# Kernel tuning notes

Hardware: AMD Instinct MI355X
Metric: run time of the kernel (lower is better)

Reference implementation:

```python
import jax, jax.numpy as jnp
import numpy as np

NCE_T = 0.07


def setup_inputs() -> dict:
    key = jax.random.key(0)
    k1, k2, k3 = jax.random.split(key, 3)
    features_1 = jax.random.normal(k1, (1, 20000, 256), dtype=jnp.float32)
    features_2 = jax.random.normal(k2, (1, 8192, 256), dtype=jnp.float32)
    map21 = jax.random.randint(k3, (8192,), 0, 20000, dtype=jnp.int64)
    return {"features_1": features_1, "features_2": features_2, "map21": map21}


def reference(features_1, features_2, map21):
    # squeeze leading batch dim (module assumes batch size 1)
    f1 = features_1[0]  # [N1, D]
    f2 = features_2[0]  # [P, D]  (P == nce_num_pairs == len(map21) -> arange branch)
    query = f1[map21]   # [P, D] gather
    keys = f2           # [P, D]
    # pairwise Euclidean distance via matmul trick (matches torch.cdist p=2)
    q_sq = jnp.sum(query * query, axis=-1)  # [P]
    k_sq = jnp.sum(keys * keys, axis=-1)    # [P]
    sq_dist = q_sq[:, None] + k_sq[None, :] - 2.0 * (query @ keys.T)  # [P, P]
    dist = jnp.sqrt(jnp.maximum(sq_dist, 0.0))
    logits = -dist / NCE_T
    # cross entropy with labels = arange(P): mean of -log_softmax diagonal
    logp = jax.nn.log_softmax(logits, axis=-1)
    loss = -jnp.mean(jnp.diagonal(logp))
    return loss
```

## Files before the change

kernel.cpp:

```cpp
#include <hip/hip_runtime.h>
#include <hip/hip_bf16.h>

#define PP      8192
#define DIM     256
#define DIMP    272
#define NKF     17
#define GS      (32 * DIMP)
#define NCHUNK  16
#define TCOLS   16
#define ROWBLK  256
#define NROWBLK (PP / ROWBLK)
#define TILEB   (32 * DIMP * 2)
#define NBUF    2

typedef __bf16 bf16_t;
using bf16x8 = __attribute__((ext_vector_type(8))) __bf16;
using bf16x4 = __attribute__((ext_vector_type(4))) __bf16;
using f32x4  = __attribute__((ext_vector_type(4))) float;
using f32x16 = __attribute__((ext_vector_type(16))) float;

typedef __attribute__((address_space(1))) void as1_void;
typedef __attribute__((address_space(3))) void as3_void;

#define C2    20.609929155556618
#define MEXP  (-340.0f)
#define COEF  ((float)(-(C2 * 1.4142135623730951) * 8388608.0))
#define KBIAS ((float)((127.0 + 340.0) * 8388608.0))
#define LN2   0.6931471805599453f

__global__ __launch_bounds__(256) void nce_prep(
    const float* __restrict__ f1, const float* __restrict__ f2,
    const int* __restrict__ map,
    bf16_t* __restrict__ qb2, bf16_t* __restrict__ kb2,
    float* __restrict__ diag2, float* __restrict__ part_l,
    unsigned* __restrict__ cnt, float* __restrict__ out)
{
    const int tid  = threadIdx.x;
    const int wave = tid >> 6, lane = tid & 63;
    const int p    = blockIdx.x * 4 + wave;
    const int gtid = blockIdx.x * 256 + tid;

    if (gtid < PP) part_l[gtid] = 0.0f;
    if (gtid < NROWBLK) cnt[gtid] = 0u;
    if (gtid == 0) out[0] = 0.0f;

    const int idx = map[p];
    const f32x4 qv = *(const f32x4*)(f1 + (size_t)idx * DIM + lane * 4);
    const f32x4 kv = *(const f32x4*)(f2 + (size_t)p * DIM + lane * 4);

    float qs = qv[0]*qv[0] + qv[1]*qv[1] + qv[2]*qv[2] + qv[3]*qv[3];
    float ks = kv[0]*kv[0] + kv[1]*kv[1] + kv[2]*kv[2] + kv[3]*kv[3];
    const f32x4 dv = qv - kv;
    float ds = dv[0]*dv[0] + dv[1]*dv[1] + dv[2]*dv[2] + dv[3]*dv[3];

    bf16x4 qo, ko;
    #pragma unroll
    for (int i = 0; i < 4; ++i) { qo[i] = (bf16_t)qv[i]; ko[i] = (bf16_t)kv[i]; }

    const int G = p >> 5, l31 = p & 31;
    const int kk = lane >> 2, h = (lane >> 1) & 1, j0 = (lane & 1) * 4;
    const size_t base = (size_t)G * GS;
    const size_t off  = base + (size_t)(kk * 64 + h * 32 + l31) * 8 + j0;
    *(bf16x4*)(qb2 + off) = qo;
    *(bf16x4*)(kb2 + off) = ko;

    #pragma unroll
    for (int s = 32; s > 0; s >>= 1) {
        qs += __shfl_xor(qs, s);
        ks += __shfl_xor(ks, s);
        ds += __shfl_xor(ds, s);
    }

    if (lane < 4) {
        const int hh = lane & 1;
        bf16x8 v;
        #pragma unroll
        for (int i = 0; i < 8; ++i) v[i] = (bf16_t)0.0f;
        if (lane == 0) {
            const float qh = -0.5f * qs;
            const bf16_t q1 = (bf16_t)qh;
            v[0] = q1; v[1] = (bf16_t)(qh - (float)q1);
            v[2] = (bf16_t)1.0f; v[3] = (bf16_t)1.0f;
        } else if (lane == 2) {
            const float kh = -0.5f * ks;
            const bf16_t k1 = (bf16_t)kh;
            v[0] = (bf16_t)1.0f; v[1] = (bf16_t)1.0f;
            v[2] = k1; v[3] = (bf16_t)(kh - (float)k1);
        }
        bf16_t* dstp = (lane < 2) ? qb2 : kb2;
        *(bf16x8*)(dstp + base + (size_t)(1024 + hh * 32 + l31) * 8) = v;
    }
    if (lane == 0)
        diag2[p] = (float)(-C2) * __builtin_amdgcn_sqrtf(ds);
}

__device__ __forceinline__ void stage(const bf16_t* __restrict__ kb2,
                                      int Gc, int wave, int lane, char* dst)
{
    __builtin_assume(wave >= 0 && wave < 4);
    __builtin_assume(lane >= 0 && lane < 64);
    const bf16_t* src = kb2 + (size_t)Gc * GS + wave * 512 + lane * 8;
    char* d = dst + wave * 1024;
    #pragma unroll
    for (int j = 0; j < 4; ++j)
        __builtin_amdgcn_global_load_lds((const as1_void*)(src + j * 2048),
                                         (as3_void*)(d + j * 4096), 16, 0, 0);
    if (wave == 0)
        __builtin_amdgcn_global_load_lds((const as1_void*)(src + 4 * 2048),
                                         (as3_void*)(d + 4 * 4096), 16, 0, 0);
}

#define PHASE(NW, DOPRE, T)                                                    \
  do {                                                                         \
    asm volatile("s_waitcnt lgkmcnt(0)\n\ts_barrier" ::: "memory");            \
    if (DOPRE) stage(kb2, c0g + (T) + 1, wave, lane, smem[((T) + 1) & 1]);     \
    asm volatile("s_waitcnt vmcnt(%c0)" :: "i"(NW) : "memory");                \
    const bf16_t* bp = (const bf16_t*)smem[(T) & 1] + lane * 8;                \
    f32x16 acc0 = {0,0,0,0,0,0,0,0,0,0,0,0,0,0,0,0};                          \
    f32x16 acc1 = {0,0,0,0,0,0,0,0,0,0,0,0,0,0,0,0};                          \
    __builtin_amdgcn_s_setprio(1);                                             \
    _Pragma("unroll")                                                          \
    for (int kk = 0; kk < NKF; ++kk) {                                         \
        const bf16x8 b = *(const bf16x8*)(bp + kk * 512);                      \
        acc0 = __builtin_amdgcn_mfma_f32_32x32x16_bf16(a0[kk], b, acc0,0,0,0); \
        acc1 = __builtin_amdgcn_mfma_f32_32x32x16_bf16(a1[kk], b, acc1,0,0,0); \
    }                                                                          \
    __builtin_amdgcn_s_setprio(0);                                             \
         \
    _Pragma("unroll")                                                          \
    for (int i = 0; i < 16; ++i) {                                             \
        const float t0 = __builtin_amdgcn_sqrtf(-acc0[i]);                     \
        const float u0 = fmaxf(fmaf(t0, COEF, KBIAS), 0.0f);                   \
        l0[i] += __uint_as_float((unsigned)u0);                                \
        const float t1 = __builtin_amdgcn_sqrtf(-acc1[i]);                     \
        const float u1 = fmaxf(fmaf(t1, COEF, KBIAS), 0.0f);                   \
        l1[i] += __uint_as_float((unsigned)u1);                                \
    }                                                                          \
  } while (0)

__global__ __launch_bounds__(256, 2) void nce_main(
    const bf16_t* __restrict__ qb2, const bf16_t* __restrict__ kb2,
    const float* __restrict__ diag2, float* __restrict__ part_l,
    unsigned* __restrict__ cnt, float* __restrict__ out)
{
    const int tid  = threadIdx.x, wave = tid >> 6, lane = tid & 63;
    const int l31  = lane & 31, h = lane >> 5;

    const int lin = blockIdx.x + (blockIdx.y << 5);
    const int xcd = lin & 7, idx = lin >> 3;
    const int rb  = (xcd & 3) * 8 + (idx & 7);
    const int cy  = (xcd >> 2) * 8 + (idx >> 3);
    const int G0  = rb * 8 + wave * 2;
    const int c0g = cy * TCOLS;

    __shared__ __align__(16) char smem[NBUF][TILEB];
    __shared__ int s_last;
    __shared__ float red[4];

    stage(kb2, c0g, wave, lane, smem[0]);

    bf16x8 a0[NKF], a1[NKF];
    {
        const bf16_t* ap0 = qb2 + (size_t)G0 * GS + lane * 8;
        const bf16_t* ap1 = ap0 + GS;
        #pragma unroll
        for (int kk = 0; kk < NKF; ++kk) {
            a0[kk] = *(const bf16x8*)(ap0 + kk * 512);
            a1[kk] = *(const bf16x8*)(ap1 + kk * 512);
        }
    }

    float l0[16], l1[16];
    #pragma unroll
    for (int i = 0; i < 16; ++i) { l0[i] = 0.0f; l1[i] = 0.0f; }

    #pragma unroll 1
    for (int t = 0; t < TCOLS - 1; ++t)
        PHASE(4, true, t);
    PHASE(0, false, TCOLS - 1);

    #pragma unroll
    for (int s = 1; s < 32; s <<= 1) {
        #pragma unroll
        for (int i = 0; i < 16; ++i) {
            l0[i] += __shfl_xor(l0[i], s);
            l1[i] += __shfl_xor(l1[i], s);
        }
    }

    if (l31 == 0) {
        #pragma unroll
        for (int i = 0; i < 16; ++i) {
            const int r = (i & 3) + 8 * (i >> 2) + 4 * h;
            atomicAdd(&part_l[G0 * 32 + r], l0[i]);
            atomicAdd(&part_l[(G0 + 1) * 32 + r], l1[i]);
        }
    }

    __syncthreads();
    if (tid == 0) {
        __threadfence();
        s_last = (atomicAdd(&cnt[rb], 1u) == NCHUNK - 1) ? 1 : 0;
    }
    __syncthreads();
    if (s_last) {
        const int row = rb * ROWBLK + tid;
        const float lf = atomicAdd(&part_l[row], 0.0f);
        float v = MEXP + __builtin_amdgcn_logf(lf) - diag2[row];
        #pragma unroll
        for (int s = 1; s < 64; s <<= 1) v += __shfl_xor(v, s);
        if (lane == 0) red[wave] = v;
        __syncthreads();
        if (tid == 0)
            atomicAdd(out, (red[0] + red[1] + red[2] + red[3]) * (LN2 / (float)PP));
    }
}

extern "C" void kernel_launch(void* const* d_in, const int* in_sizes, int n_in,
                              void* d_out, int out_size, void* d_ws, size_t ws_size,
                              hipStream_t stream)
{
    const float* f1  = (const float*)d_in[0];
    const float* f2  = (const float*)d_in[1];
    const int*   map = (const int*)d_in[2];
    float* out = (float*)d_out;

    char* ws = (char*)d_ws;
    bf16_t*   qb2    = (bf16_t*)ws;
    bf16_t*   kb2    = qb2 + (size_t)256 * GS;
    float*    diag2  = (float*)(ws + 2ull * 256 * GS * sizeof(bf16_t));
    float*    part_l = diag2 + PP;
    unsigned* cnt    = (unsigned*)(part_l + PP);

    nce_prep<<<PP / 4, 256, 0, stream>>>(f1, f2, map, qb2, kb2, diag2,
                                         part_l, cnt, out);
    nce_main<<<dim3(NROWBLK, NCHUNK), 256, 0, stream>>>(qb2, kb2, diag2,
                                                        part_l, cnt, out);
}
```

Before: 120.3 us.

## Software-pipeline MFMA and epilogue across tiles with split accumulators

Restructures the column-tile loop so the MFMA chain for tile t runs in the same phase as the sqrt/softmax epilogue of tile t-1, using double-buffered accumulator sets. Each tile's K reduction is split into even and odd accumulator chains to shorten the MFMA dependency chain, and the two chains are summed in the epilogue. Launch bounds drop to one block per SIMD group to make room for the extra accumulator registers. The cost is a much higher register footprint, lower occupancy, and a full vmcnt(0) wait at each barrier instead of a partial one.

```diff
diff --git a/kernel.cpp b/kernel.cpp
--- a/kernel.cpp
+++ b/kernel.cpp
@@ -110,35 +110,49 @@
                                          (as3_void*)(d + 4 * 4096), 16, 0, 0);
 }
 
-#define PHASE(NW, DOPRE, T)                                                    \
+#define PH_MFMA(T, Pe0, Po0, Pe1, Po1)                                         \
   do {                                                                         \
-    asm volatile("s_waitcnt lgkmcnt(0)\n\ts_barrier" ::: "memory");            \
-    if (DOPRE) stage(kb2, c0g + (T) + 1, wave, lane, smem[((T) + 1) & 1]);     \
-    asm volatile("s_waitcnt vmcnt(%c0)" :: "i"(NW) : "memory");                \
     const bf16_t* bp = (const bf16_t*)smem[(T) & 1] + lane * 8;                \
-    f32x16 acc0 = {0,0,0,0,0,0,0,0,0,0,0,0,0,0,0,0};                          \
-    f32x16 acc1 = {0,0,0,0,0,0,0,0,0,0,0,0,0,0,0,0};                          \
+    bf16x8 be = *(const bf16x8*)(bp);                                          \
+    bf16x8 bo = *(const bf16x8*)(bp + 512);                                    \
     __builtin_amdgcn_s_setprio(1);                                             \
+    Pe0 = __builtin_amdgcn_mfma_f32_32x32x16_bf16(a0[0], be, ZZ, 0, 0, 0);     \
+    Pe1 = __builtin_amdgcn_mfma_f32_32x32x16_bf16(a1[0], be, ZZ, 0, 0, 0);     \
+    Po0 = __builtin_amdgcn_mfma_f32_32x32x16_bf16(a0[1], bo, ZZ, 0, 0, 0);     \
+    Po1 = __builtin_amdgcn_mfma_f32_32x32x16_bf16(a1[1], bo, ZZ, 0, 0, 0);     \
     _Pragma("unroll")                                                          \
-    for (int kk = 0; kk < NKF; ++kk) {                                         \
-        const bf16x8 b = *(const bf16x8*)(bp + kk * 512);                      \
-        acc0 = __builtin_amdgcn_mfma_f32_32x32x16_bf16(a0[kk], b, acc0,0,0,0); \
-        acc1 = __builtin_amdgcn_mfma_f32_32x32x16_bf16(a1[kk], b, acc1,0,0,0); \
+    for (int kk = 2; kk < NKF; kk += 2) {                                      \
+        be = *(const bf16x8*)(bp + kk * 512);                                  \
+        Pe0 = __builtin_amdgcn_mfma_f32_32x32x16_bf16(a0[kk], be, Pe0,0,0,0);  \
+        Pe1 = __builtin_amdgcn_mfma_f32_32x32x16_bf16(a1[kk], be, Pe1,0,0,0);  \
+        if (kk + 1 < NKF) {                                                    \
+            bo = *(const bf16x8*)(bp + (kk + 1) * 512);                        \
+            Po0 = __builtin_amdgcn_mfma_f32_32x32x16_bf16(a0[kk+1], bo, Po0,0,0,0); \
+            Po1 = __builtin_amdgcn_mfma_f32_32x32x16_bf16(a1[kk+1], bo, Po1,0,0,0); \
+        }                                                                      \
     }                                                                          \
     __builtin_amdgcn_s_setprio(0);                                             \
-         \
+  } while (0)
+
+#define EPI(Pe0, Po0, Pe1, Po1)                                                \
+  do {                                                                         \
     _Pragma("unroll")                                                          \
     for (int i = 0; i < 16; ++i) {                                             \
-        const float t0 = __builtin_amdgcn_sqrtf(-acc0[i]);                     \
+        const float s0 = Pe0[i] + Po0[i];                                      \
+        const float t0 = __builtin_amdgcn_sqrtf(-s0);                          \
         const float u0 = fmaxf(fmaf(t0, COEF, KBIAS), 0.0f);                   \
         l0[i] += __uint_as_float((unsigned)u0);                                \
-        const float t1 = __builtin_amdgcn_sqrtf(-acc1[i]);                     \
+        const float s1 = Pe1[i] + Po1[i];                                      \
+        const float t1 = __builtin_amdgcn_sqrtf(-s1);                          \
         const float u1 = fmaxf(fmaf(t1, COEF, KBIAS), 0.0f);                   \
         l1[i] += __uint_as_float((unsigned)u1);                                \
     }                                                                          \
   } while (0)
 
-__global__ __launch_bounds__(256, 2) void nce_main(
+#define PH_BOT() \
+    asm volatile("s_waitcnt vmcnt(0) lgkmcnt(0)\n\ts_barrier" ::: "memory")
+
+__global__ __launch_bounds__(256, 1) void nce_main(
     const bf16_t* __restrict__ qb2, const bf16_t* __restrict__ kb2,
     const float* __restrict__ diag2, float* __restrict__ part_l,
     unsigned* __restrict__ cnt, float* __restrict__ out)
@@ -174,10 +188,30 @@
     #pragma unroll
     for (int i = 0; i < 16; ++i) { l0[i] = 0.0f; l1[i] = 0.0f; }
 
+    const f32x16 ZZ = {0,0,0,0,0,0,0,0,0,0,0,0,0,0,0,0};
+    f32x16 pe0, po0, pe1, po1;
+    f32x16 qe0, qo0, qe1, qo1;
+
+    PH_BOT();
+
+    stage(kb2, c0g + 1, wave, lane, smem[1]);
+    PH_MFMA(0, pe0, po0, pe1, po1);
+    PH_BOT();
+
     #pragma unroll 1
-    for (int t = 0; t < TCOLS - 1; ++t)
-        PHASE(4, true, t);
-    PHASE(0, false, TCOLS - 1);
+    for (int tt = 1; tt <= 13; tt += 2) {
+        stage(kb2, c0g + tt + 1, wave, lane, smem[(tt + 1) & 1]);
+        PH_MFMA(tt, qe0, qo0, qe1, qo1);
+        EPI(pe0, po0, pe1, po1);
+        PH_BOT();
+        stage(kb2, c0g + tt + 2, wave, lane, smem[tt & 1]);
+        PH_MFMA(tt + 1, pe0, po0, pe1, po1);
+        EPI(qe0, qo0, qe1, qo1);
+        PH_BOT();
+    }
+    PH_MFMA(15, qe0, qo0, qe1, qo1);
+    EPI(pe0, po0, pe1, po1);
+    EPI(qe0, qo0, qe1, qo1);
 
     #pragma unroll
     for (int s = 1; s < 32; s <<= 1) {
```

Measured after the change: 131.0 us. +8.9%, slower.

## Software-pipeline MFMA tiles with deferred epilogue and split even/odd accumulators

Applied to the files above, without the earlier changes.

Restructures each column-tile phase so that the sqrt/clamp epilogue for the previous tile runs interleaved between MFMA groups of the current tile. It also splits each accumulator into even and odd chains to shorten MFMA dependency chains, and prefetches B fragments from LDS in batches. The waitcnt/barrier moves to the end of each phase. Launch bounds drop to one block per CU so the doubled accumulator registers fit, which trades occupancy for instruction-level parallelism.

```diff
diff --git a/kernel.cpp b/kernel.cpp
--- a/kernel.cpp
+++ b/kernel.cpp
@@ -110,35 +110,68 @@
                                          (as3_void*)(d + 4 * 4096), 16, 0, 0);
 }
 
-#define PHASE(NW, DOPRE, T)                                                    \
-  do {                                                                         \
-    asm volatile("s_waitcnt lgkmcnt(0)\n\ts_barrier" ::: "memory");            \
-    if (DOPRE) stage(kb2, c0g + (T) + 1, wave, lane, smem[((T) + 1) & 1]);     \
-    asm volatile("s_waitcnt vmcnt(%c0)" :: "i"(NW) : "memory");                \
-    const bf16_t* bp = (const bf16_t*)smem[(T) & 1] + lane * 8;                \
-    f32x16 acc0 = {0,0,0,0,0,0,0,0,0,0,0,0,0,0,0,0};                          \
-    f32x16 acc1 = {0,0,0,0,0,0,0,0,0,0,0,0,0,0,0,0};                          \
-    __builtin_amdgcn_s_setprio(1);                                             \
+#define PH_BOT() \
+    asm volatile("s_waitcnt vmcnt(0) lgkmcnt(0)\n\ts_barrier" ::: "memory")
+
+#define LDB(dst, kkidx) dst = *(const bf16x8*)(bp + (kkidx) * 512)
+
+#define MQZ(B0,B1,B2,B3, CE0,CO0,CE1,CO1)                                      \
+    CE0 = __builtin_amdgcn_mfma_f32_32x32x16_bf16(a0[0], B0, ZZ, 0,0,0);       \
+    CE1 = __builtin_amdgcn_mfma_f32_32x32x16_bf16(a1[0], B0, ZZ, 0,0,0);       \
+    CO0 = __builtin_amdgcn_mfma_f32_32x32x16_bf16(a0[1], B1, ZZ, 0,0,0);       \
+    CO1 = __builtin_amdgcn_mfma_f32_32x32x16_bf16(a1[1], B1, ZZ, 0,0,0);       \
+    CE0 = __builtin_amdgcn_mfma_f32_32x32x16_bf16(a0[2], B2, CE0, 0,0,0);      \
+    CE1 = __builtin_amdgcn_mfma_f32_32x32x16_bf16(a1[2], B2, CE1, 0,0,0);      \
+    CO0 = __builtin_amdgcn_mfma_f32_32x32x16_bf16(a0[3], B3, CO0, 0,0,0);      \
+    CO1 = __builtin_amdgcn_mfma_f32_32x32x16_bf16(a1[3], B3, CO1, 0,0,0);
+
+#define MQ(K0, B0,B1,B2,B3, CE0,CO0,CE1,CO1)                                   \
+    CE0 = __builtin_amdgcn_mfma_f32_32x32x16_bf16(a0[(K0)+0], B0, CE0, 0,0,0); \
+    CE1 = __builtin_amdgcn_mfma_f32_32x32x16_bf16(a1[(K0)+0], B0, CE1, 0,0,0); \
+    CO0 = __builtin_amdgcn_mfma_f32_32x32x16_bf16(a0[(K0)+1], B1, CO0, 0,0,0); \
+    CO1 = __builtin_amdgcn_mfma_f32_32x32x16_bf16(a1[(K0)+1], B1, CO1, 0,0,0); \
+    CE0 = __builtin_amdgcn_mfma_f32_32x32x16_bf16(a0[(K0)+2], B2, CE0, 0,0,0); \
+    CE1 = __builtin_amdgcn_mfma_f32_32x32x16_bf16(a1[(K0)+2], B2, CE1, 0,0,0); \
+    CO0 = __builtin_amdgcn_mfma_f32_32x32x16_bf16(a0[(K0)+3], B3, CO0, 0,0,0); \
+    CO1 = __builtin_amdgcn_mfma_f32_32x32x16_bf16(a1[(K0)+3], B3, CO1, 0,0,0);
+
+#define EPIS(S, E0,O0,E1,O1)                                                   \
     _Pragma("unroll")                                                          \
-    for (int kk = 0; kk < NKF; ++kk) {                                         \
-        const bf16x8 b = *(const bf16x8*)(bp + kk * 512);                      \
-        acc0 = __builtin_amdgcn_mfma_f32_32x32x16_bf16(a0[kk], b, acc0,0,0,0); \
-        acc1 = __builtin_amdgcn_mfma_f32_32x32x16_bf16(a1[kk], b, acc1,0,0,0); \
-    }                                                                          \
-    __builtin_amdgcn_s_setprio(0);                                             \
-         \
-    _Pragma("unroll")                                                          \
-    for (int i = 0; i < 16; ++i) {                                             \
-        const float t0 = __builtin_amdgcn_sqrtf(-acc0[i]);                     \
+    for (int i = 4*(S); i < 4*(S)+4; ++i) {                                    \
+        const float s0 = E0[i] + O0[i];                                        \
+        const float t0 = __builtin_amdgcn_sqrtf(-s0);                          \
         const float u0 = fmaxf(fmaf(t0, COEF, KBIAS), 0.0f);                   \
         l0[i] += __uint_as_float((unsigned)u0);                                \
-        const float t1 = __builtin_amdgcn_sqrtf(-acc1[i]);                     \
+        const float s1 = E1[i] + O1[i];                                        \
+        const float t1 = __builtin_amdgcn_sqrtf(-s1);                          \
         const float u1 = fmaxf(fmaf(t1, COEF, KBIAS), 0.0f);                   \
         l1[i] += __uint_as_float((unsigned)u1);                                \
-    }                                                                          \
+    }
+
+#define PHASE(T, CE0,CO0,CE1,CO1, PE0,PO0,PE1,PO1, DO_EPI, DOPRE)              \
+  do {                                                                         \
+    if (DOPRE) stage(kb2, c0g + (T) + 1, wave, lane, smem[((T) + 1) & 1]);     \
+    const bf16_t* bp = (const bf16_t*)smem[(T) & 1] + lane * 8;                \
+    bf16x8 bA0, bA1, bA2, bA3, bB0, bB1, bB2, bB3;                             \
+    LDB(bA0, 0); LDB(bA1, 1); LDB(bA2, 2); LDB(bA3, 3);                        \
+    LDB(bB0, 4); LDB(bB1, 5); LDB(bB2, 6); LDB(bB3, 7);                        \
+    MQZ(bA0,bA1,bA2,bA3, CE0,CO0,CE1,CO1);                                     \
+    if (DO_EPI) { EPIS(0, PE0,PO0,PE1,PO1); }                                  \
+    LDB(bA0, 8); LDB(bA1, 9); LDB(bA2, 10); LDB(bA3, 11);                      \
+    MQ(4, bB0,bB1,bB2,bB3, CE0,CO0,CE1,CO1);                                   \
+    if (DO_EPI) { EPIS(1, PE0,PO0,PE1,PO1); }                                  \
+    LDB(bB0, 12); LDB(bB1, 13); LDB(bB2, 14); LDB(bB3, 15);                    \
+    MQ(8, bA0,bA1,bA2,bA3, CE0,CO0,CE1,CO1);                                   \
+    if (DO_EPI) { EPIS(2, PE0,PO0,PE1,PO1); }                                  \
+    LDB(bA0, 16);                                                              \
+    MQ(12, bB0,bB1,bB2,bB3, CE0,CO0,CE1,CO1);                                  \
+    if (DO_EPI) { EPIS(3, PE0,PO0,PE1,PO1); }                                  \
+    CE0 = __builtin_amdgcn_mfma_f32_32x32x16_bf16(a0[16], bA0, CE0, 0,0,0);    \
+    CE1 = __builtin_amdgcn_mfma_f32_32x32x16_bf16(a1[16], bA0, CE1, 0,0,0);    \
+    PH_BOT();                                                                  \
   } while (0)
 
-__global__ __launch_bounds__(256, 2) void nce_main(
+__global__ __launch_bounds__(256, 1) void nce_main(
     const bf16_t* __restrict__ qb2, const bf16_t* __restrict__ kb2,
     const float* __restrict__ diag2, float* __restrict__ part_l,
     unsigned* __restrict__ cnt, float* __restrict__ out)
@@ -174,10 +207,24 @@
     #pragma unroll
     for (int i = 0; i < 16; ++i) { l0[i] = 0.0f; l1[i] = 0.0f; }
 
+    const f32x16 ZZ = {0,0,0,0,0,0,0,0,0,0,0,0,0,0,0,0};
+    f32x16 pe0, po0, pe1, po1;
+    f32x16 qe0, qo0, qe1, qo1;
+
+    PH_BOT();
+
+    PHASE(0, pe0,po0,pe1,po1, qe0,qo0,qe1,qo1, false, true);
+
     #pragma unroll 1
-    for (int t = 0; t < TCOLS - 1; ++t)
-        PHASE(4, true, t);
-    PHASE(0, false, TCOLS - 1);
+    for (int tt = 1; tt <= 13; tt += 2) {
+        PHASE(tt,     qe0,qo0,qe1,qo1, pe0,po0,pe1,po1, true, true);
+        PHASE(tt + 1, pe0,po0,pe1,po1, qe0,qo0,qe1,qo1, true, true);
+    }
+    PHASE(15, qe0,qo0,qe1,qo1, pe0,po0,pe1,po1, true, false);
+    EPIS(0, qe0,qo0,qe1,qo1);
+    EPIS(1, qe0,qo0,qe1,qo1);
+    EPIS(2, qe0,qo0,qe1,qo1);
+    EPIS(3, qe0,qo0,qe1,qo1);
 
     #pragma unroll
     for (int s = 1; s < 32; s <<= 1) {
```

Measured after the change: 127.8 us. +6.3%, slower.

## Double rows per wave to four MFMA tiles with register-prefetched B operand

Applied to the files above, without the earlier changes.

Each wave now holds four 32-row query tiles in registers instead of two, so the row block grows to 512 and the grid halves. Each B fragment read from shared memory is therefore reused across four MFMAs. The B fragment for the next k step is loaded one iteration ahead, and the barrier moves to the end of each phase with a full vmcnt wait. Occupancy drops to one block per SIMD set, which leaves less latency hiding and fewer blocks than CUs, and the launch-side grid change is not visible.

```diff
diff --git a/kernel.cpp b/kernel.cpp
--- a/kernel.cpp
+++ b/kernel.cpp
@@ -8,7 +8,7 @@
 #define GS      (32 * DIMP)
 #define NCHUNK  16
 #define TCOLS   16
-#define ROWBLK  256
+#define ROWBLK  512
 #define NROWBLK (PP / ROWBLK)
 #define TILEB   (32 * DIMP * 2)
 #define NBUF    2
@@ -110,35 +110,41 @@
                                          (as3_void*)(d + 4 * 4096), 16, 0, 0);
 }
 
-#define PHASE(NW, DOPRE, T)                                                    \
+#define PHASE(DOPRE, T)                                                        \
   do {                                                                         \
-    asm volatile("s_waitcnt lgkmcnt(0)\n\ts_barrier" ::: "memory");            \
     if (DOPRE) stage(kb2, c0g + (T) + 1, wave, lane, smem[((T) + 1) & 1]);     \
-    asm volatile("s_waitcnt vmcnt(%c0)" :: "i"(NW) : "memory");                \
     const bf16_t* bp = (const bf16_t*)smem[(T) & 1] + lane * 8;                \
     f32x16 acc0 = {0,0,0,0,0,0,0,0,0,0,0,0,0,0,0,0};                          \
     f32x16 acc1 = {0,0,0,0,0,0,0,0,0,0,0,0,0,0,0,0};                          \
-    __builtin_amdgcn_s_setprio(1);                                             \
+    f32x16 acc2 = {0,0,0,0,0,0,0,0,0,0,0,0,0,0,0,0};                          \
+    f32x16 acc3 = {0,0,0,0,0,0,0,0,0,0,0,0,0,0,0,0};                          \
+    bf16x8 bc = *(const bf16x8*)bp;                                            \
     _Pragma("unroll")                                                          \
     for (int kk = 0; kk < NKF; ++kk) {                                         \
-        const bf16x8 b = *(const bf16x8*)(bp + kk * 512);                      \
-        acc0 = __builtin_amdgcn_mfma_f32_32x32x16_bf16(a0[kk], b, acc0,0,0,0); \
-        acc1 = __builtin_amdgcn_mfma_f32_32x32x16_bf16(a1[kk], b, acc1,0,0,0); \
+        const bf16x8 bn = (kk + 1 < NKF)                                       \
+            ? *(const bf16x8*)(bp + (kk + 1) * 512) : bc;                      \
+        acc0 = __builtin_amdgcn_mfma_f32_32x32x16_bf16(a0[kk], bc, acc0,0,0,0);\
+        acc1 = __builtin_amdgcn_mfma_f32_32x32x16_bf16(a1[kk], bc, acc1,0,0,0);\
+        acc2 = __builtin_amdgcn_mfma_f32_32x32x16_bf16(a2[kk], bc, acc2,0,0,0);\
+        acc3 = __builtin_amdgcn_mfma_f32_32x32x16_bf16(a3[kk], bc, acc3,0,0,0);\
+        bc = bn;                                                               \
     }                                                                          \
-    __builtin_amdgcn_s_setprio(0);                                             \
          \
     _Pragma("unroll")                                                          \
     for (int i = 0; i < 16; ++i) {                                             \
         const float t0 = __builtin_amdgcn_sqrtf(-acc0[i]);                     \
-        const float u0 = fmaxf(fmaf(t0, COEF, KBIAS), 0.0f);                   \
-        l0[i] += __uint_as_float((unsigned)u0);                                \
+        l0[i] += __uint_as_float((unsigned)fmaxf(fmaf(t0, COEF, KBIAS), 0.0f));\
         const float t1 = __builtin_amdgcn_sqrtf(-acc1[i]);                     \
-        const float u1 = fmaxf(fmaf(t1, COEF, KBIAS), 0.0f);                   \
-        l1[i] += __uint_as_float((unsigned)u1);                                \
+        l1[i] += __uint_as_float((unsigned)fmaxf(fmaf(t1, COEF, KBIAS), 0.0f));\
+        const float t2 = __builtin_amdgcn_sqrtf(-acc2[i]);                     \
+        l2[i] += __uint_as_float((unsigned)fmaxf(fmaf(t2, COEF, KBIAS), 0.0f));\
+        const float t3 = __builtin_amdgcn_sqrtf(-acc3[i]);                     \
+        l3[i] += __uint_as_float((unsigned)fmaxf(fmaf(t3, COEF, KBIAS), 0.0f));\
     }                                                                          \
+    asm volatile("s_waitcnt vmcnt(0) lgkmcnt(0)\n\ts_barrier" ::: "memory");   \
   } while (0)
 
-__global__ __launch_bounds__(256, 2) void nce_main(
+__global__ __launch_bounds__(256, 1) void nce_main(
     const bf16_t* __restrict__ qb2, const bf16_t* __restrict__ kb2,
     const float* __restrict__ diag2, float* __restrict__ part_l,
     unsigned* __restrict__ cnt, float* __restrict__ out)
@@ -146,11 +152,11 @@
     const int tid  = threadIdx.x, wave = tid >> 6, lane = tid & 63;
     const int l31  = lane & 31, h = lane >> 5;
 
-    const int lin = blockIdx.x + (blockIdx.y << 5);
+    const int lin = blockIdx.x + (blockIdx.y << 4);
     const int xcd = lin & 7, idx = lin >> 3;
-    const int rb  = (xcd & 3) * 8 + (idx & 7);
-    const int cy  = (xcd >> 2) * 8 + (idx >> 3);
-    const int G0  = rb * 8 + wave * 2;
+    const int rb  = (xcd & 3) * 4 + (idx & 3);
+    const int cy  = (xcd >> 2) * 8 + (idx >> 2);
+    const int G0  = rb * 16 + wave * 4;
     const int c0g = cy * TCOLS;
 
     __shared__ __align__(16) char smem[NBUF][TILEB];
@@ -159,25 +165,28 @@
 
     stage(kb2, c0g, wave, lane, smem[0]);
 
-    bf16x8 a0[NKF], a1[NKF];
+    bf16x8 a0[NKF], a1[NKF], a2[NKF], a3[NKF];
     {
-        const bf16_t* ap0 = qb2 + (size_t)G0 * GS + lane * 8;
-        const bf16_t* ap1 = ap0 + GS;
+        const bf16_t* ap = qb2 + (size_t)G0 * GS + lane * 8;
         #pragma unroll
         for (int kk = 0; kk < NKF; ++kk) {
-            a0[kk] = *(const bf16x8*)(ap0 + kk * 512);
-            a1[kk] = *(const bf16x8*)(ap1 + kk * 512);
-        }
-    }
-
-    float l0[16], l1[16];
-    #pragma unroll
-    for (int i = 0; i < 16; ++i) { l0[i] = 0.0f; l1[i] = 0.0f; }
+            a0[kk] = *(const bf16x8*)(ap + kk * 512);
+            a1[kk] = *(const bf16x8*)(ap + GS + kk * 512);
+            a2[kk] = *(const bf16x8*)(ap + 2 * GS + kk * 512);
+            a3[kk] = *(const bf16x8*)(ap + 3 * GS + kk * 512);
+        }
+    }
+
+    float l0[16], l1[16], l2[16], l3[16];
+    #pragma unroll
+    for (int i = 0; i < 16; ++i) { l0[i]=0.0f; l1[i]=0.0f; l2[i]=0.0f; l3[i]=0.0f; }
+
+    asm volatile("s_waitcnt vmcnt(0) lgkmcnt(0)\n\ts_barrier" ::: "memory");
 
     #pragma unroll 1
     for (int t = 0; t < TCOLS - 1; ++t)
-        PHASE(4, true, t);
-    PHASE(0, false, TCOLS - 1);
+        PHASE(true, t);
+    PHASE(false, TCOLS - 1);
 
     #pragma unroll
     for (int s = 1; s < 32; s <<= 1) {
@@ -185,6 +194,8 @@
         for (int i = 0; i < 16; ++i) {
             l0[i] += __shfl_xor(l0[i], s);
             l1[i] += __shfl_xor(l1[i], s);
+            l2[i] += __shfl_xor(l2[i], s);
+            l3[i] += __shfl_xor(l3[i], s);
         }
     }
 
@@ -192,8 +203,10 @@
         #pragma unroll
         for (int i = 0; i < 16; ++i) {
             const int r = (i & 3) + 8 * (i >> 2) + 4 * h;
-            atomicAdd(&part_l[G0 * 32 + r], l0[i]);
+            atomicAdd(&part_l[(G0 + 0) * 32 + r], l0[i]);
             atomicAdd(&part_l[(G0 + 1) * 32 + r], l1[i]);
+            atomicAdd(&part_l[(G0 + 2) * 32 + r], l2[i]);
+            atomicAdd(&part_l[(G0 + 3) * 32 + r], l3[i]);
         }
     }
 
@@ -204,9 +217,12 @@
     }
     __syncthreads();
     if (s_last) {
-        const int row = rb * ROWBLK + tid;
-        const float lf = atomicAdd(&part_l[row], 0.0f);
-        float v = MEXP + __builtin_amdgcn_logf(lf) - diag2[row];
+        const int rowA = rb * ROWBLK + tid;
+        const int rowB = rowA + 256;
+        const float lfA = atomicAdd(&part_l[rowA], 0.0f);
+        const float lfB = atomicAdd(&part_l[rowB], 0.0f);
+        float v = (MEXP + __builtin_amdgcn_logf(lfA) - diag2[rowA])
+                + (MEXP + __builtin_amdgcn_logf(lfB) - diag2[rowB]);
         #pragma unroll
         for (int s = 1; s < 64; s <<= 1) v += __shfl_xor(v, s);
         if (lane == 0) red[wave] = v;
```

Measured after the change: 128.3 us. 1.07x slower.
